# Performance work log

Hardware: AMD Instinct MI355X
Metric: run time of the kernel (lower is better)

Reference implementation:

```python
import jax, jax.numpy as jnp
import numpy as np

EPS = 1e-18

_SOBEL_H = jnp.array([[-1., -2., -1.], [0., 0., 0.], [1., 2., 1.]], dtype=jnp.float32)


def _sobel_mag(x, eps):
    # x: [B,1,H,W]; depth-1 3x3 conv with 'same' padding, two fixed kernels
    wh = _SOBEL_H.reshape(1, 1, 3, 3).astype(x.dtype)   # horizontal kernel
    wv = _SOBEL_H.T.reshape(1, 1, 3, 3).astype(x.dtype)  # vertical kernel
    dn = jax.lax.conv_dimension_numbers(x.shape, wh.shape, ('NCHW', 'OIHW', 'NCHW'))
    gv = jax.lax.conv_general_dilated(x, wv, (1, 1), 'SAME', dimension_numbers=dn)
    gh = jax.lax.conv_general_dilated(x, wh, (1, 1), 'SAME', dimension_numbers=dn)
    return jnp.sqrt(gv * gv + gh * gh + eps)


def setup_inputs() -> dict:
    key = jax.random.key(0)
    k1, k2 = jax.random.split(key)
    shape = (64, 1, 512, 512)
    y_p = jax.random.uniform(k1, shape, dtype=jnp.float32)
    y_t = jax.random.uniform(k2, shape, dtype=jnp.float32)
    return {"y_p": y_p, "y_t": y_t}


def reference(y_p, y_t):
    eps = EPS
    ypg = _sobel_mag(y_p, eps)
    ytg = _sobel_mag(y_t, eps)
    out = (ytg - ypg) ** 2
    mask = (out == 0.0).astype(out.dtype)
    out = out + mask * eps
    out = jnp.sqrt(out + eps) * (1.0 - mask)
    return jnp.mean(out)
```

## Files before the change

### kernel.cpp

```cpp
#include <hip/hip_runtime.h>

#define IMG_W 512
#define IMG_H 512
#define BATCH 64
#define TILE_W 64
#define TILE_H 32
#define LDS_STRIDE 72
#define LDS_ROWS 34
#define TILES_X (IMG_W / TILE_W)
#define TILES_Y (IMG_H / TILE_H)
#define NBLOCKS (BATCH * TILES_X * TILES_Y)
#define NPIX (BATCH * IMG_W * IMG_H)

__device__ __forceinline__ float fast_sqrtf(float x) {
    return __builtin_amdgcn_sqrtf(x);
}

__global__ __launch_bounds__(256, 8) void sobel_loss_kernel(
    const float* __restrict__ yp, const float* __restrict__ yt,
    float* __restrict__ bsums)
{
    __shared__ __align__(16) float ldsP[LDS_ROWS * LDS_STRIDE];
    __shared__ __align__(16) float ldsT[LDS_ROWS * LDS_STRIDE];
    __shared__ float wred[4];

    const int tid = threadIdx.x;
    const int bid = blockIdx.x;
    const int b    = bid >> 7;
    const int tile = bid & 127;
    const int ty0 = (tile >> 3) * TILE_H;
    const int tx0 = (tile & 7) * TILE_W;

    const float* __restrict__ imgp = yp + (size_t)b * (IMG_W * IMG_H);
    const float* __restrict__ imgt = yt + (size_t)b * (IMG_W * IMG_H);

    for (int li = tid; li < LDS_ROWS * 18; li += 256) {
        int r = li / 18;
        int q = li - r * 18;
        int gy = ty0 - 1 + r;
        int gx = tx0 - 4 + (q << 2);
        float4 vp = {0.f, 0.f, 0.f, 0.f};
        float4 vt = {0.f, 0.f, 0.f, 0.f};
        if (gy >= 0 && gy < IMG_H) {
            const float* rowp = imgp + (size_t)gy * IMG_W;
            const float* rowt = imgt + (size_t)gy * IMG_W;
            if (gx >= 0 && gx + 3 < IMG_W) {
                vp = *(const float4*)(rowp + gx);
                vt = *(const float4*)(rowt + gx);
            } else {
                float* ep = &vp.x;
                float* et = &vt.x;
#pragma unroll
                for (int e = 0; e < 4; ++e) {
                    int x = gx + e;
                    if (x >= 0 && x < IMG_W) {
                        ep[e] = rowp[x];
                        et[e] = rowt[x];
                    }
                }
            }
        }
        *(float4*)(&ldsP[r * LDS_STRIDE + (q << 2)]) = vp;
        *(float4*)(&ldsT[r * LDS_STRIDE + (q << 2)]) = vt;
    }
    __syncthreads();

    const int px  = (tid & 15) << 2;
    const int ry0 = (tid >> 4) << 1;

    float hp[3][6], ht[3][6];
    float sp[3][4], st[3][4];

    auto load_row = [&](int slot, int lr) {
        const float* rp = &ldsP[lr * LDS_STRIDE + px];
        const float* rt = &ldsT[lr * LDS_STRIDE + px];
        float4 v4p = *(const float4*)(rp + 4);
        float4 v4t = *(const float4*)(rt + 4);
        hp[slot][0] = rp[3]; hp[slot][1] = v4p.x; hp[slot][2] = v4p.y;
        hp[slot][3] = v4p.z; hp[slot][4] = v4p.w; hp[slot][5] = rp[8];
        ht[slot][0] = rt[3]; ht[slot][1] = v4t.x; ht[slot][2] = v4t.y;
        ht[slot][3] = v4t.z; ht[slot][4] = v4t.w; ht[slot][5] = rt[8];
#pragma unroll
        for (int j = 0; j < 4; ++j) {
            sp[slot][j] = fmaf(2.f, hp[slot][j + 1], hp[slot][j]) + hp[slot][j + 2];
            st[slot][j] = fmaf(2.f, ht[slot][j + 1], ht[slot][j]) + ht[slot][j + 2];
        }
    };

    load_row(0, ry0);
    load_row(1, ry0 + 1);

    float lsum = 0.f;
#pragma unroll
    for (int i = 0; i < 2; ++i) {
        const int s0 = i % 3, s1 = (i + 1) % 3, s2 = (i + 2) % 3;
        load_row(s2, ry0 + 2 + i);

        float cp[6], ct[6];
#pragma unroll
        for (int k = 0; k < 6; ++k) {
            cp[k] = fmaf(2.f, hp[s1][k], hp[s0][k]) + hp[s2][k];
            ct[k] = fmaf(2.f, ht[s1][k], ht[s0][k]) + ht[s2][k];
        }
#pragma unroll
        for (int j = 0; j < 4; ++j) {
            float ghp = sp[s2][j] - sp[s0][j];
            float gvp = cp[j + 2] - cp[j];
            float magp = fast_sqrtf(fmaf(gvp, gvp, fmaf(ghp, ghp, 1e-18f)));
            float ght = st[s2][j] - st[s0][j];
            float gvt = ct[j + 2] - ct[j];
            float magt = fast_sqrtf(fmaf(gvt, gvt, fmaf(ght, ght, 1e-18f)));
            lsum += fabsf(magt - magp);
        }
    }

#pragma unroll
    for (int off = 32; off > 0; off >>= 1)
        lsum += __shfl_down(lsum, off, 64);
    const int lane = tid & 63, wid = tid >> 6;
    if (lane == 0) wred[wid] = lsum;
    __syncthreads();
    if (tid == 0)
        bsums[bid] = wred[0] + wred[1] + wred[2] + wred[3];
}

__global__ __launch_bounds__(256) void reduce_final(
    const float* __restrict__ bsums, float* __restrict__ out)
{
    __shared__ float wred[4];
    const int tid = threadIdx.x;
    float s = 0.f;
    for (int i = tid; i < NBLOCKS; i += 256) s += bsums[i];
#pragma unroll
    for (int off = 32; off > 0; off >>= 1)
        s += __shfl_down(s, off, 64);
    if ((tid & 63) == 0) wred[tid >> 6] = s;
    __syncthreads();
    if (tid == 0)
        out[0] = (wred[0] + wred[1] + wred[2] + wred[3]) * (1.0f / (float)NPIX);
}

__global__ void zero_out_kernel(float* out) { out[0] = 0.f; }

__global__ __launch_bounds__(256, 8) void sobel_loss_kernel_atomic(
    const float* __restrict__ yp, const float* __restrict__ yt,
    float* __restrict__ out, float inv_n);

extern "C" void kernel_launch(void* const* d_in, const int* in_sizes, int n_in,
                              void* d_out, int out_size, void* d_ws, size_t ws_size,
                              hipStream_t stream) {
    const float* yp = (const float*)d_in[0];
    const float* yt = (const float*)d_in[1];
    float* out = (float*)d_out;

    float* bsums = (float*)d_ws;
    sobel_loss_kernel<<<NBLOCKS, 256, 0, stream>>>(yp, yt, bsums);
    reduce_final<<<1, 256, 0, stream>>>(bsums, out);
}
```

Baseline: 155.1 us.

## Replace LDS tiling with per-wave full-row streaming and shuffle halos

The kernel drops the shared-memory tile and instead gives each wave a full 512-pixel image row (8 pixels per lane), streaming 8 rows per wave down a 3-row register window. Horizontal neighbours come from cross-lane shuffles rather than LDS reads. This removes LDS staging, the block barrier and most of the halo reloading. The costs are a 1/8 vertical halo re-read from global memory, more registers (occupancy hint lowered to 4), fewer blocks (1024), and extra row sums computed inside the loop.

```diff
diff --git a/kernel.cpp b/kernel.cpp
--- a/kernel.cpp
+++ b/kernel.cpp
@@ -3,113 +3,91 @@
 #define IMG_W 512
 #define IMG_H 512
 #define BATCH 64
-#define TILE_W 64
-#define TILE_H 32
-#define LDS_STRIDE 72
-#define LDS_ROWS 34
-#define TILES_X (IMG_W / TILE_W)
-#define TILES_Y (IMG_H / TILE_H)
-#define NBLOCKS (BATCH * TILES_X * TILES_Y)
+#define ROWS_PER_WAVE 8
+#define WAVES_PER_BLOCK 4
+#define ROWS_PER_BLOCK (ROWS_PER_WAVE * WAVES_PER_BLOCK)
+#define SLABS (IMG_H / ROWS_PER_BLOCK)
+#define NBLOCKS (BATCH * SLABS)
 #define NPIX (BATCH * IMG_W * IMG_H)
 
 __device__ __forceinline__ float fast_sqrtf(float x) {
     return __builtin_amdgcn_sqrtf(x);
 }
 
-__global__ __launch_bounds__(256, 8) void sobel_loss_kernel(
+__global__ __launch_bounds__(256, 4) void sobel_loss_kernel(
     const float* __restrict__ yp, const float* __restrict__ yt,
     float* __restrict__ bsums)
 {
-    __shared__ __align__(16) float ldsP[LDS_ROWS * LDS_STRIDE];
-    __shared__ __align__(16) float ldsT[LDS_ROWS * LDS_STRIDE];
-    __shared__ float wred[4];
+    __shared__ float wred[WAVES_PER_BLOCK];
 
-    const int tid = threadIdx.x;
-    const int bid = blockIdx.x;
-    const int b    = bid >> 7;
-    const int tile = bid & 127;
-    const int ty0 = (tile >> 3) * TILE_H;
-    const int tx0 = (tile & 7) * TILE_W;
+    const int tid  = threadIdx.x;
+    const int lane = tid & 63;
+    const int wv   = tid >> 6;
+    const int bid  = blockIdx.x;
+    const int b    = bid >> 4;
+    const int slab = bid & (SLABS - 1);
+    const int y0   = slab * ROWS_PER_BLOCK + wv * ROWS_PER_WAVE;
+    const int x0   = lane << 3;
 
     const float* __restrict__ imgp = yp + (size_t)b * (IMG_W * IMG_H);
     const float* __restrict__ imgt = yt + (size_t)b * (IMG_W * IMG_H);
 
-    for (int li = tid; li < LDS_ROWS * 18; li += 256) {
-        int r = li / 18;
-        int q = li - r * 18;
-        int gy = ty0 - 1 + r;
-        int gx = tx0 - 4 + (q << 2);
-        float4 vp = {0.f, 0.f, 0.f, 0.f};
-        float4 vt = {0.f, 0.f, 0.f, 0.f};
-        if (gy >= 0 && gy < IMG_H) {
-            const float* rowp = imgp + (size_t)gy * IMG_W;
-            const float* rowt = imgt + (size_t)gy * IMG_W;
-            if (gx >= 0 && gx + 3 < IMG_W) {
-                vp = *(const float4*)(rowp + gx);
-                vt = *(const float4*)(rowt + gx);
-            } else {
-                float* ep = &vp.x;
-                float* et = &vt.x;
-#pragma unroll
-                for (int e = 0; e < 4; ++e) {
-                    int x = gx + e;
-                    if (x >= 0 && x < IMG_W) {
-                        ep[e] = rowp[x];
-                        et[e] = rowt[x];
-                    }
-                }
-            }
+    float hp[3][10], ht[3][10];
+
+    auto load_row = [&](int slot, int y) {
+        float4 ap = {0.f, 0.f, 0.f, 0.f}, bp = {0.f, 0.f, 0.f, 0.f};
+        float4 at = {0.f, 0.f, 0.f, 0.f}, bt = {0.f, 0.f, 0.f, 0.f};
+        if (y >= 0 && y < IMG_H) {
+            const float* rp = imgp + (size_t)y * IMG_W + x0;
+            const float* rt = imgt + (size_t)y * IMG_W + x0;
+            ap = *(const float4*)rp;
+            bp = *(const float4*)(rp + 4);
+            at = *(const float4*)rt;
+            bt = *(const float4*)(rt + 4);
         }
-        *(float4*)(&ldsP[r * LDS_STRIDE + (q << 2)]) = vp;
-        *(float4*)(&ldsT[r * LDS_STRIDE + (q << 2)]) = vt;
-    }
-    __syncthreads();
-
-    const int px  = (tid & 15) << 2;
-    const int ry0 = (tid >> 4) << 1;
-
-    float hp[3][6], ht[3][6];
-    float sp[3][4], st[3][4];
-
-    auto load_row = [&](int slot, int lr) {
-        const float* rp = &ldsP[lr * LDS_STRIDE + px];
-        const float* rt = &ldsT[lr * LDS_STRIDE + px];
-        float4 v4p = *(const float4*)(rp + 4);
-        float4 v4t = *(const float4*)(rt + 4);
-        hp[slot][0] = rp[3]; hp[slot][1] = v4p.x; hp[slot][2] = v4p.y;
-        hp[slot][3] = v4p.z; hp[slot][4] = v4p.w; hp[slot][5] = rp[8];
-        ht[slot][0] = rt[3]; ht[slot][1] = v4t.x; ht[slot][2] = v4t.y;
-        ht[slot][3] = v4t.z; ht[slot][4] = v4t.w; ht[slot][5] = rt[8];
-#pragma unroll
-        for (int j = 0; j < 4; ++j) {
-            sp[slot][j] = fmaf(2.f, hp[slot][j + 1], hp[slot][j]) + hp[slot][j + 2];
-            st[slot][j] = fmaf(2.f, ht[slot][j + 1], ht[slot][j]) + ht[slot][j + 2];
-        }
+        float lp = __shfl_up(bp.w, 1, 64);
+        float rp_ = __shfl_down(ap.x, 1, 64);
+        float lt = __shfl_up(bt.w, 1, 64);
+        float rt_ = __shfl_down(at.x, 1, 64);
+        if (lane == 0)  { lp = 0.f; lt = 0.f; }
+        if (lane == 63) { rp_ = 0.f; rt_ = 0.f; }
+        hp[slot][0] = lp;   ht[slot][0] = lt;
+        hp[slot][1] = ap.x; hp[slot][2] = ap.y; hp[slot][3] = ap.z; hp[slot][4] = ap.w;
+        hp[slot][5] = bp.x; hp[slot][6] = bp.y; hp[slot][7] = bp.z; hp[slot][8] = bp.w;
+        ht[slot][1] = at.x; ht[slot][2] = at.y; ht[slot][3] = at.z; ht[slot][4] = at.w;
+        ht[slot][5] = bt.x; ht[slot][6] = bt.y; ht[slot][7] = bt.z; ht[slot][8] = bt.w;
+        hp[slot][9] = rp_;  ht[slot][9] = rt_;
     };
 
-    load_row(0, ry0);
-    load_row(1, ry0 + 1);
+    load_row(0, y0 - 1);
+    load_row(1, y0);
 
     float lsum = 0.f;
 #pragma unroll
-    for (int i = 0; i < 2; ++i) {
+    for (int i = 0; i < ROWS_PER_WAVE; ++i) {
         const int s0 = i % 3, s1 = (i + 1) % 3, s2 = (i + 2) % 3;
-        load_row(s2, ry0 + 2 + i);
+        load_row(s2, y0 + 1 + i);
 
-        float cp[6], ct[6];
+        float cp[10], ct[10];
 #pragma unroll
-        for (int k = 0; k < 6; ++k) {
+        for (int k = 0; k < 10; ++k) {
             cp[k] = fmaf(2.f, hp[s1][k], hp[s0][k]) + hp[s2][k];
             ct[k] = fmaf(2.f, ht[s1][k], ht[s0][k]) + ht[s2][k];
         }
 #pragma unroll
-        for (int j = 0; j < 4; ++j) {
-            float ghp = sp[s2][j] - sp[s0][j];
+        for (int j = 0; j < 8; ++j) {
+            float tp  = fmaf(2.f, hp[s2][j + 1], hp[s2][j]) + hp[s2][j + 2];
+            float bp_ = fmaf(2.f, hp[s0][j + 1], hp[s0][j]) + hp[s0][j + 2];
+            float ghp = tp - bp_;
             float gvp = cp[j + 2] - cp[j];
             float magp = fast_sqrtf(fmaf(gvp, gvp, fmaf(ghp, ghp, 1e-18f)));
-            float ght = st[s2][j] - st[s0][j];
+
+            float tt  = fmaf(2.f, ht[s2][j + 1], ht[s2][j]) + ht[s2][j + 2];
+            float bt_ = fmaf(2.f, ht[s0][j + 1], ht[s0][j]) + ht[s0][j + 2];
+            float ght = tt - bt_;
             float gvt = ct[j + 2] - ct[j];
             float magt = fast_sqrtf(fmaf(gvt, gvt, fmaf(ght, ght, 1e-18f)));
+
             lsum += fabsf(magt - magp);
         }
     }
@@ -117,8 +95,7 @@
 #pragma unroll
     for (int off = 32; off > 0; off >>= 1)
         lsum += __shfl_down(lsum, off, 64);
-    const int lane = tid & 63, wid = tid >> 6;
-    if (lane == 0) wred[wid] = lsum;
+    if (lane == 0) wred[wv] = lsum;
     __syncthreads();
     if (tid == 0)
         bsums[bid] = wred[0] + wred[1] + wred[2] + wred[3];
@@ -140,12 +117,6 @@
         out[0] = (wred[0] + wred[1] + wred[2] + wred[3]) * (1.0f / (float)NPIX);
 }
 
-__global__ void zero_out_kernel(float* out) { out[0] = 0.f; }
-
-__global__ __launch_bounds__(256, 8) void sobel_loss_kernel_atomic(
-    const float* __restrict__ yp, const float* __restrict__ yt,
-    float* __restrict__ out, float inv_n);
-
 extern "C" void kernel_launch(void* const* d_in, const int* in_sizes, int n_in,
                               void* d_out, int out_size, void* d_ws, size_t ws_size,
                               hipStream_t stream) {
```

Result: slower. 203.5 us (+31.2%).
